# Optimization experiments

Hardware: AMD Instinct MI355X
Metric: run time of the kernel (lower is better)

The kernel has to match this reference:

```python
import jax, jax.numpy as jnp
import numpy as np

B, P, N0 = 8, 32, 10000
K, HIDP = 8, 4
HIDR = 4 * K * HIDP + K   # 136 = backbone output channels
HEADS = 2
E = 160000


def _conv_bn(x, w, b, g, be, dil):
    # x: [B,1,P,N0]; w: [k,1,ks,1]; valid conv along time with dilation dil, then BatchNorm2d (batch stats)
    y = jax.lax.conv_general_dilated(x, w, (1, 1), 'VALID', rhs_dilation=(dil, 1),
                                     dimension_numbers=('NCHW', 'OIHW', 'NCHW'))
    y = y + b[None, :, None, None]
    mu = jnp.mean(y, axis=(0, 2, 3), keepdims=True)
    var = jnp.var(y, axis=(0, 2, 3), keepdims=True)
    return g[None, :, None, None] * (y - mu) * jax.lax.rsqrt(var + 1e-5) + be[None, :, None, None]


def _branch(x, w, b, g, be, dil, pool):
    y = _conv_bn(x, w, b, g, be, dil)
    if pool:  # AdaptiveMaxPool2d((HIDP, N0)): pools only the time axis (node axis already N0)
        T = y.shape[2]
        y = jnp.stack([jnp.max(y[:, :, (i * T) // HIDP: -((-(i + 1) * T) // HIDP), :], axis=2)
                       for i in range(HIDP)], axis=2)
    return y.reshape(y.shape[0], -1, y.shape[-1])  # [B, k*hidP or k, N0]


def _backbone(x, pl1, pl2, pp1, pp2, pg):
    x = x.reshape(-1, 1, P, N0)
    parts = [_branch(x, *pl1, 1, True), _branch(x, *pl2, 1, True),   # local: ks 3,5 dil 1
             _branch(x, *pp1, 2, True), _branch(x, *pp2, 2, True),   # periodic: ks 3,5 dil 2
             _branch(x, *pg, 1, False)]                               # global: ks P, no pool
    return jnp.tanh(jnp.concatenate(parts, axis=1).transpose(0, 2, 1))  # [B, N0, HIDR]


def _gat(xn, W, a_src, a_dst, bias, src, dst, heads, out_ch):
    # PyG GATConv: linear (no bias) -> per-head additive attention -> segment softmax over dst -> scatter-sum
    n = xn.shape[0]
    h = (xn @ W).reshape(n, heads, out_ch)                              # [N,H,C]
    al = jax.nn.leaky_relu(jnp.sum(h * a_src, -1)[src] + jnp.sum(h * a_dst, -1)[dst], 0.2)  # [E',H]
    amax = jax.ops.segment_max(al, dst, num_segments=n)
    ex = jnp.exp(al - amax[dst])
    coef = ex / (jax.ops.segment_sum(ex, dst, num_segments=n)[dst] + 1e-16)
    out = jax.ops.segment_sum(coef[:, :, None] * h[src], dst, num_segments=n)  # [N,H,C]
    return out.reshape(n, heads * out_ch) + bias


def setup_inputs() -> dict:
    key = jax.random.key(0)
    ks = iter(jax.random.split(key, 64))
    nrm = lambda *s: jax.random.normal(next(ks), s, jnp.float32) * 0.05
    d = {"x": jax.random.normal(next(ks), (B, P, N0), jnp.float32)}
    for nm, ksz in (("l1", 3), ("l2", 5), ("p1", 3), ("p2", 5), ("g", P)):
        d["w_" + nm] = nrm(K, 1, ksz, 1)
        d["b_" + nm] = nrm(K)
        d["g_" + nm] = jnp.ones((K,), jnp.float32)
        d["be_" + nm] = jnp.zeros((K,), jnp.float32)
    d["W1"] = nrm(HIDR, HEADS * HIDR); d["as1"] = nrm(HEADS, HIDR); d["ad1"] = nrm(HEADS, HIDR); d["bb1"] = nrm(HEADS * HIDR)
    d["W2"] = nrm(HEADS * HIDR, HIDR); d["as2"] = nrm(1, HIDR); d["ad2"] = nrm(1, HIDR); d["bb2"] = nrm(HIDR)
    d["Wo"] = nrm(2 * HIDR, HIDR); d["bo"] = nrm(HIDR)
    d["Wo2"] = nrm(HIDR, 1); d["bo2"] = nrm(1)
    d["edge_index"] = jax.random.randint(next(ks), (2, E), 0, N0, jnp.int32)
    return d


def reference(x, w_l1, b_l1, g_l1, be_l1, w_l2, b_l2, g_l2, be_l2,
              w_p1, b_p1, g_p1, be_p1, w_p2, b_p2, g_p2, be_p2,
              w_g, b_g, g_g, be_g,
              W1, as1, ad1, bb1, W2, as2, ad2, bb2, Wo, bo, Wo2, bo2, edge_index):
    feat = _backbone(x, (w_l1, b_l1, g_l1, be_l1), (w_l2, b_l2, g_l2, be_l2),
                     (w_p1, b_p1, g_p1, be_p1), (w_p2, b_p2, g_p2, be_p2),
                     (w_g, b_g, g_g, be_g))                                  # [B,N0,HIDR]
    loop = jnp.arange(N0, dtype=edge_index.dtype)                            # GATConv add_self_loops=True
    src = jnp.concatenate([edge_index[0], loop])
    dst = jnp.concatenate([edge_index[1], loop])
    # original loops GATConv per batch item over shared edge_index; vmap is the batched equivalent
    g1 = jax.vmap(lambda f: _gat(f, W1, as1, ad1, bb1, src, dst, HEADS, HIDR))(feat)  # [B,N0,2*HIDR]
    g2 = jax.vmap(lambda f: _gat(f, W2, as2, ad2, bb2, src, dst, 1, HIDR))(g1)        # [B,N0,HIDR]
    ns = jax.nn.leaky_relu(jnp.concatenate([g2, feat], axis=-1))             # dropout is identity at eval
    res = jax.nn.leaky_relu(ns @ Wo + bo)
    return (res @ Wo2 + bo2)[..., 0]                                         # [B,N0]
```

## Files before the change

kernel.cpp:

```cpp
#include <hip/hip_runtime.h>
#include <hip/hip_bf16.h>
#include <math.h>

typedef unsigned short u16;
typedef unsigned int   u32;
typedef short v8s __attribute__((ext_vector_type(8)));
typedef float v4f __attribute__((ext_vector_type(4)));
typedef float v2f __attribute__((ext_vector_type(2)));
#define DEV static __device__ __forceinline__

DEV float u2f(u16 u){ union{u32 i; float f;} v; v.i = ((u32)u)<<16; return v.f; }
DEV u16   f2u(float f){ union{float ff; u32 i;} v; v.ff = f; u32 r = v.i + 0x7fffu + ((v.i>>16)&1u); return (u16)(r>>16); }
DEV float lrelu02(float x){ return x > 0.f ? x : 0.2f*x; }
DEV float lrelu01(float x){ return x > 0.f ? x : 0.01f*x; }
DEV float fast_tanh(float x){
  float cx = fminf(fmaxf(x, -15.f), 15.f);
  float e = __expf(2.f*cx);
  return (e - 1.f) * __builtin_amdgcn_rcpf(e + 1.f);
}
DEV float wred_sum(float v){
  #pragma unroll
  for (int o = 32; o > 0; o >>= 1) v += __shfl_xor(v, o, 64);
  return v;
}
DEV float wred_max32(float v){
  #pragma unroll
  for (int o = 16; o > 0; o >>= 1) v = fmaxf(v, __shfl_xor(v, o, 64));
  return v;
}
DEV float wred_sum32(float v){
  #pragma unroll
  for (int o = 16; o > 0; o >>= 1) v += __shfl_xor(v, o, 64);
  return v;
}
DEV v2f unpack2(u32 w){
  v2f r;
  r.x = __uint_as_float(w << 16);
  r.y = __uint_as_float(w & 0xffff0000u);
  return r;
}

constexpr int B_   = 8;
constexpr int P_   = 32;
constexpr int N0_  = 10000;
constexpr int NODES = B_ * N0_;
constexpr int E_   = 160000;
constexpr int NE_  = E_ + N0_;

__global__ void __launch_bounds__(256) k_setup(int* __restrict__ zbase,
    const float* __restrict__ Wo, u16* __restrict__ WoT,
    const float* __restrict__ W1, const float* __restrict__ W2, u16* __restrict__ W12T,
    const float* __restrict__ as1, const float* __restrict__ ad1,
    float* __restrict__ va1s, float* __restrict__ va1d,
    const float* __restrict__ as2, const float* __restrict__ ad2,
    const float* __restrict__ bb1,
    float* __restrict__ v2ss, float* __restrict__ v2dd,
    float* __restrict__ cc, float* __restrict__ b12)
{
  __shared__ float l2s[272], l2d[272];
  int blk = blockIdx.x, tid = threadIdx.x;
  if (blk < 79){ int i = blk*256 + tid; if (i < 20080) zbase[i] = 0; return; }
  blk -= 79;
  if (blk < 180){
    int i = blk*256 + tid; if (i >= 144*320) return;
    int n = i/320, k = i - n*320; float v = 0.f;
    if (n < 136){
      if (k < 136) v = Wo[(size_t)k*136 + n];
      else if (k >= 160 && k < 296) v = Wo[(size_t)(k-24)*136 + n];
    }
    WoT[i] = f2u(v); return;
  }
  blk -= 180;
  if (blk < 162){
    int i = blk*256 + tid; if (i >= 144*288) return;
    int n = i/288, kk = i - n*288; float v = 0.f;
    if (n < 136 && kk < 272){
      int hh = kk/136, k = kk - hh*136;
      for (int c = 0; c < 136; c++)
        v = fmaf(W1[(size_t)k*272 + hh*136 + c], W2[(size_t)(hh*136+c)*136 + n], v);
    }
    W12T[i] = f2u(v); return;
  }
  blk -= 162;
  if (blk < 2){
    int t = blk*256 + tid; if (t >= 272) return;
    int hh = t/136, k = t - hh*136; float s = 0.f, d = 0.f;
    for (int c = 0; c < 136; c++){
      float w = W1[(size_t)k*272 + hh*136 + c];
      s = fmaf(w, as1[hh*136+c], s);
      d = fmaf(w, ad1[hh*136+c], d);
    }
    va1s[t] = s; va1d[t] = d; return;
  }
  blk -= 2;
  {
    for (int m = tid; m < 272; m += 256){
      float vs = 0.f, vd = 0.f;
      for (int n2 = 0; n2 < 136; n2++){
        float w2 = W2[(size_t)m*136 + n2];
        vs = fmaf(w2, as2[n2], vs);
        vd = fmaf(w2, ad2[n2], vd);
      }
      l2s[m] = vs; l2d[m] = vd;
    }
    __syncthreads();
    int t0 = blk*256 + tid;
    if (t0 < 272){
      int hh = t0/136, k = t0 - hh*136; float s = 0.f, d = 0.f;
      for (int c = 0; c < 136; c++){
        float w = W1[(size_t)k*272 + hh*136 + c];
        s = fmaf(w, l2s[hh*136+c], s);
        d = fmaf(w, l2d[hh*136+c], d);
      }
      v2ss[t0] = s; v2dd[t0] = d;
    }
    if (blk == 1){
      if (tid < 64){
        float s = 0.f, d = 0.f;
        for (int m = tid; m < 272; m += 64){
          s = fmaf(bb1[m], l2s[m], s);
          d = fmaf(bb1[m], l2d[m], d);
        }
        s = wred_sum(s); d = wred_sum(d);
        if (tid == 0){ cc[0] = s; cc[1] = d; }
      } else if (tid < 200){
        int n2 = tid - 64; float v = 0.f;
        for (int m = 0; m < 272; m++) v = fmaf(bb1[m], W2[(size_t)m*136 + n2], v);
        b12[n2] = v;
      }
    }
  }
}

DEV void load_convw(float* lw, const float* wl1, const float* wl2, const float* wp1,
                    const float* wp2, const float* wg, int tid, int nth){
  for (int i = tid; i < 384; i += nth){
    float v;
    if      (i < 24)  v = wl1[i];
    else if (i < 64)  v = wl2[i-24];
    else if (i < 88)  v = wp1[i-64];
    else if (i < 128) v = wp2[i-88];
    else              v = wg [i-128];
    lw[i] = v;
  }
}

template<int KS,int DIL,int T>
DEV void conv_stats(const float* xc, const float* wk, float& s, float& q){
  #pragma unroll
  for (int t = 0; t < T; t++){
    float v = 0.f;
    #pragma unroll
    for (int j = 0; j < KS; j++) v = fmaf(wk[j], xc[t + j*DIL], v);
    s += v; q = fmaf(v, v, q);
  }
}

__global__ void __launch_bounds__(256) k_bn_stats(
    const float* __restrict__ x,
    const float* __restrict__ wl1, const float* __restrict__ wl2,
    const float* __restrict__ wp1, const float* __restrict__ wp2,
    const float* __restrict__ wg,
    float* __restrict__ gsum, float* __restrict__ gsq)
{
  __shared__ float lw[384];
  __shared__ float lacc[80];
  const int tid = threadIdx.x;
  load_convw(lw, wl1, wl2, wp1, wp2, wg, tid, 256);
  if (tid < 80) lacc[tid] = 0.f;
  __syncthreads();

  const int lane = tid & 63, wv = tid >> 6;
  const int nodeLocal = (wv >> 1)*64 + lane;
  const int half = wv & 1;
  const int gid = blockIdx.x*128 + nodeLocal;
  float xc[P_];
  if (gid < NODES){
    int b = gid / N0_, n = gid - b*N0_;
    const float* xp = x + (size_t)b*P_*N0_ + n;
    #pragma unroll
    for (int p = 0; p < P_; p++) xc[p] = xp[(size_t)p*N0_];
  } else {
    #pragma unroll
    for (int p = 0; p < P_; p++) xc[p] = 0.f;
  }

  auto red = [&](int ch, float s, float q){
    #pragma unroll
    for (int o = 32; o > 0; o >>= 1){ s += __shfl_down(s,o,64); q += __shfl_down(q,o,64); }
    if (lane == 0){ atomicAdd(&lacc[ch], s); atomicAdd(&lacc[40+ch], q); }
  };

  if (half == 0){
    #pragma unroll
    for (int k = 0; k < 8; k++){ float s=0,q=0; conv_stats<3,1,30>(xc, lw      + k*3 , s,q); red(k,     s,q); }
    #pragma unroll
    for (int k = 0; k < 8; k++){ float s=0,q=0; conv_stats<5,1,28>(xc, lw + 24 + k*5 , s,q); red(8+k,   s,q); }
  } else {
    #pragma unroll
    for (int k = 0; k < 8; k++){ float s=0,q=0; conv_stats<3,2,28>(xc, lw + 64 + k*3 , s,q); red(16+k,  s,q); }
    #pragma unroll
    for (int k = 0; k < 8; k++){ float s=0,q=0; conv_stats<5,2,24>(xc, lw + 88 + k*5 , s,q); red(24+k,  s,q); }
    #pragma unroll
    for (int k = 0; k < 8; k++){ float s=0,q=0; conv_stats<32,1,1>(xc, lw + 128+ k*32, s,q); red(32+k,  s,q); }
  }

  __syncthreads();
  if (tid < 40)      atomicAdd(&gsum[tid],    lacc[tid]);
  else if (tid < 80) atomicAdd(&gsq [tid-40], lacc[tid]);
}

__global__ void k_count(const int* __restrict__ ei, int* __restrict__ counts,
                        const float* __restrict__ gsum, const float* __restrict__ gsq,
                        float* __restrict__ sA, float* __restrict__ sB,
                        const float* g0, const float* g1, const float* g2, const float* g3, const float* g4,
                        const float* e0, const float* e1, const float* e2, const float* e3, const float* e4){
  if (blockIdx.x == 665){
    int t = threadIdx.x;
    if (t >= 40) return;
    int bi = t >> 3, k = t & 7;
    const int Ts[5] = {30,28,28,24,1};
    float cnt  = (float)NODES * (float)Ts[bi];
    float mean = gsum[t] / cnt;
    float var  = gsq[t] / cnt - mean*mean;
    const float* gp = bi==0?g0: bi==1?g1: bi==2?g2: bi==3?g3: g4;
    const float* ep = bi==0?e0: bi==1?e1: bi==2?e2: bi==3?e3: e4;
    float a = gp[k] * rsqrtf(fmaxf(var, 0.f) + 1e-5f);
    sA[t] = a;
    sB[t] = ep[k] - a*mean;
    return;
  }
  int e = blockIdx.x*blockDim.x + threadIdx.x;
  if (e >= NE_) return;
  int dst = (e < E_) ? ei[E_ + e] : (e - E_);
  atomicAdd(&counts[dst], 1);
}

__global__ void __launch_bounds__(1024) k_scan_perm(const int* __restrict__ counts,
                                                    int* __restrict__ offs,
                                                    int* __restrict__ perm){
  __shared__ int part[1024];
  __shared__ int hist[129];
  __shared__ int base[129];
  int t = threadIdx.x;
  if (blockIdx.x == 0){
    int loc[10]; int s = 0;
    #pragma unroll
    for (int i = 0; i < 10; i++){
      int idx = t*10 + i;
      int c = (idx < N0_) ? counts[idx] : 0;
      loc[i] = s; s += c;
    }
    part[t] = s;
    __syncthreads();
    for (int o = 1; o < 1024; o <<= 1){
      int v = (t >= o) ? part[t-o] : 0;
      __syncthreads();
      part[t] += v;
      __syncthreads();
    }
    int pre = (t == 0) ? 0 : part[t-1];
    #pragma unroll
    for (int i = 0; i < 10; i++){
      int idx = t*10 + i;
      if (idx < N0_) offs[idx] = pre + loc[i];
    }
    if (t == 0) offs[N0_] = part[1023];
  } else {
    if (t < 129) hist[t] = 0;
    __syncthreads();
    int dloc[10];
    #pragma unroll
    for (int i = 0; i < 10; i++){
      int idx = t*10 + i;
      if (idx < N0_){
        int d = min(counts[idx], 128);
        dloc[i] = d;
        atomicAdd(&hist[d], 1);
      }
    }
    __syncthreads();
    if (t == 0){
      int s = 0;
      for (int b = 0; b <= 128; b++){ base[b] = s; s += hist[b]; }
    }
    __syncthreads();
    #pragma unroll
    for (int i = 0; i < 10; i++){
      int idx = t*10 + i;
      if (idx < N0_){
        int pos = atomicAdd(&base[dloc[i]], 1);
        perm[pos] = idx;
      }
    }
  }
}

__global__ void k_scatter(const int* __restrict__ ei, const int* __restrict__ offs,
                          int* __restrict__ cursor, int* __restrict__ srcl){
  int e = blockIdx.x*blockDim.x + threadIdx.x;
  if (e >= NE_) return;
  int src, dst;
  if (e < E_){ src = ei[e]; dst = ei[E_ + e]; } else { src = dst = e - E_; }
  int pos = atomicAdd(&cursor[dst], 1);
  srcl[offs[dst] + pos] = src;
}

template<int KS,int DIL,int T>
DEV void conv_pool4(const float* xc, const float* wk, float A, float Bc, float* o4){
  float y[T];
  #pragma unroll
  for (int t = 0; t < T; t++){
    float v = 0.f;
    #pragma unroll
    for (int j = 0; j < KS; j++) v = fmaf(wk[j], xc[t + j*DIL], v);
    y[t] = fmaf(A, v, Bc);
  }
  #pragma unroll
  for (int i = 0; i < 4; i++){
    const int lo = (i*T)/4, hi = ((i+1)*T + 3)/4;
    float m = y[lo];
    #pragma unroll
    for (int t = 0; t < T; t++){ if (t > lo && t < hi) m = fmaxf(m, y[t]); }
    o4[i] = m;
  }
}

__global__ void __launch_bounds__(256) k_feat(
    const float* __restrict__ x,
    const float* __restrict__ wl1, const float* __restrict__ wl2,
    const float* __restrict__ wp1, const float* __restrict__ wp2,
    const float* __restrict__ wg,
    const float* __restrict__ sA, const float* __restrict__ sB,
    const float* __restrict__ va1s, const float* __restrict__ va1d,
    u16* __restrict__ feat, u16* __restrict__ featL,
    float* __restrict__ asrc1, float* __restrict__ adst1,
    int base, int m)
{
  __shared__ float lw[384];
  __shared__ float lA[40], lB[40];
  __shared__ float4 lv4[136];
  __shared__ float sdt[128][4];
  const int tid = threadIdx.x;
  load_convw(lw, wl1, wl2, wp1, wp2, wg, tid, 256);
  if (tid < 40){ lA[tid] = sA[tid]; lB[tid] = sB[tid]; }
  for (int i = tid; i < 136; i += 256)
    lv4[i] = make_float4(va1s[i], va1d[i], va1s[136+i], va1d[136+i]);
  __syncthreads();

  const int lane = tid & 63, wv = tid >> 6;
  const int nodeLocal = (wv >> 1)*64 + lane;
  const int half = wv & 1;
  const int nodeIdx = blockIdx.x*128 + nodeLocal;
  const bool act = nodeIdx < m;
  const int gcl = base + (act ? nodeIdx : (m-1));
  int b = gcl / N0_, n = gcl - b*N0_;
  float xc[P_];
  const float* xp = x + (size_t)b*P_*N0_ + n;
  #pragma unroll
  for (int p = 0; p < P_; p++) xc[p] = xp[(size_t)p*N0_];

  float dt[4] = {0.f,0.f,0.f,0.f};
  u32 pk[4], pkl[4];
  u16* orow  = feat  + (size_t)nodeIdx*160;
  u16* olrow = featL + (size_t)nodeIdx*160;
  auto emit = [&](int ch, float v){
    float t = fast_tanh(v);
    float4 vv = lv4[ch];
    dt[0] = fmaf(t, vv.x, dt[0]);
    dt[1] = fmaf(t, vv.y, dt[1]);
    dt[2] = fmaf(t, vv.z, dt[2]);
    dt[3] = fmaf(t, vv.w, dt[3]);
    u16 h  = f2u(t);
    u16 hl = f2u(lrelu01(t));
    int s = ch & 7;
    if ((s & 1) == 0){ pk[s>>1] = h;                pkl[s>>1] = hl; }
    else             { pk[s>>1] |= ((u32)h) << 16;  pkl[s>>1] |= ((u32)hl) << 16; }
    if (s == 7 && act){
      *(uint4*)(orow  + (ch - 7)) = make_uint4(pk[0],pk[1],pk[2],pk[3]);
      *(uint4*)(olrow + (ch - 7)) = make_uint4(pkl[0],pkl[1],pkl[2],pkl[3]);
    }
  };

  float o4[4];
  if (half == 0){
    #pragma unroll
    for (int k = 0; k < 8; k++){
      conv_pool4<3,1,30>(xc, lw + k*3, lA[k], lB[k], o4);
      #pragma unroll
      for (int i = 0; i < 4; i++) emit(k*4+i, o4[i]);
    }
    #pragma unroll
    for (int k = 0; k < 8; k++){
      conv_pool4<5,1,28>(xc, lw + 24 + k*5, lA[8+k], lB[8+k], o4);
      #pragma unroll
      for (int i = 0; i < 4; i++) emit(32 + k*4+i, o4[i]);
    }
  } else {
    #pragma unroll
    for (int k = 0; k < 8; k++){
      conv_pool4<3,2,28>(xc, lw + 64 + k*3, lA[16+k], lB[16+k], o4);
      #pragma unroll
      for (int i = 0; i < 4; i++) emit(64 + k*4+i, o4[i]);
    }
    #pragma unroll
    for (int k = 0; k < 8; k++){
      conv_pool4<5,2,24>(xc, lw + 88 + k*5, lA[24+k], lB[24+k], o4);
      #pragma unroll
      for (int i = 0; i < 4; i++) emit(96 + k*4+i, o4[i]);
    }
    #pragma unroll
    for (int k = 0; k < 8; k++){
      float v = 0.f;
      #pragma unroll
      for (int j = 0; j < 32; j++) v = fmaf(lw[128 + k*32 + j], xc[j], v);
      emit(128 + k, fmaf(lA[32+k], v, lB[32+k]));
    }
  }

  if (half == 1){
    sdt[nodeLocal][0] = dt[0]; sdt[nodeLocal][1] = dt[1];
    sdt[nodeLocal][2] = dt[2]; sdt[nodeLocal][3] = dt[3];
  }
  __syncthreads();
  if (half == 0 && act){
    asrc1[(size_t)nodeIdx*2]   = dt[0] + sdt[nodeLocal][0];
    asrc1[(size_t)nodeIdx*2+1] = dt[2] + sdt[nodeLocal][2];
    adst1[(size_t)nodeIdx*2]   = dt[1] + sdt[nodeLocal][1];
    adst1[(size_t)nodeIdx*2+1] = dt[3] + sdt[nodeLocal][3];
  }
}

template<int MT,int KT1,int KT2,int NT,int EPI,int LR2>
__global__ void __launch_bounds__(256) k_mfma(
    const u16* __restrict__ A1, int sA1,
    const u16* __restrict__ A2, int sA2,
    const u16* __restrict__ BT, int sBT,
    u16* __restrict__ C, int sC, int nbase,
    const float* __restrict__ bias, int m,
    const float* __restrict__ w2v, const float* __restrict__ bo2p, float* __restrict__ fout)
{
  const int wv = threadIdx.x >> 6, lane = threadIdx.x & 63;
  const int quad = lane >> 4, l15 = lane & 15;
  const int mb = blockIdx.x*(MT*64) + wv*(MT*16);
  int ar[MT];
  #pragma unroll
  for (int mt = 0; mt < MT; mt++) ar[mt] = min(mb + mt*16 + l15, m-1);

  v4f acc[MT][NT];
  #pragma unroll
  for (int mt = 0; mt < MT; mt++)
    #pragma unroll
    for (int nt = 0; nt < NT; nt++)
      acc[mt][nt] = (v4f){0.f,0.f,0.f,0.f};

  for (int kt = 0; kt < KT1+KT2; kt++){
    const u16* ab; int sA, koff;
    if (KT2 == 0 || kt < KT1){ ab = A1; sA = sA1; koff = kt*32; }
    else { ab = A2; sA = sA2; koff = (kt-KT1)*32; }
    v8s a[MT];
    #pragma unroll
    for (int mt = 0; mt < MT; mt++)
      a[mt] = *(const v8s*)(ab + (size_t)ar[mt]*sA + koff + quad*8);
    if (KT2 > 0 && LR2 && kt >= KT1){
      #pragma unroll
      for (int mt = 0; mt < MT; mt++)
        #pragma unroll
        for (int j = 0; j < 8; j++){
          float f = u2f((u16)a[mt][j]);
          f = f > 0.f ? f : 0.01f*f;
          a[mt][j] = (short)f2u(f);
        }
    }
    const int kb = kt*32 + quad*8;
    #pragma unroll
    for (int nt = 0; nt < NT; nt++){
      v8s b = *(const v8s*)(BT + (size_t)(nbase + nt*16 + l15)*sBT + kb);
      #pragma unroll
      for (int mt = 0; mt < MT; mt++)
        acc[mt][nt] = __builtin_amdgcn_mfma_f32_16x16x32_bf16(a[mt], b, acc[mt][nt], 0, 0, 0);
    }
  }

  if (EPI == 2){
    const float bo2v = bo2p[0];
    #pragma unroll
    for (int mt = 0; mt < MT; mt++){
      float part[4] = {0.f,0.f,0.f,0.f};
      #pragma unroll
      for (int nt = 0; nt < NT; nt++){
        const int col = nt*16 + l15;
        float wv2 = (col < 136) ? w2v[col] : 0.f;
        float bv  = bias[min(col,135)];
        #pragma unroll
        for (int i = 0; i < 4; i++){
          float xv = lrelu01(acc[mt][nt][i] + bv);
          part[i] = fmaf(xv, wv2, part[i]);
        }
      }
      #pragma unroll
      for (int i = 0; i < 4; i++){
        float v = part[i];
        v += __shfl_xor(v, 1, 64);
        v += __shfl_xor(v, 2, 64);
        v += __shfl_xor(v, 4, 64);
        v += __shfl_xor(v, 8, 64);
        int r = mb + mt*16 + quad*4 + i;
        if (l15 == 0 && r < m) fout[r] = v + bo2v;
      }
    }
    return;
  }

  #pragma unroll
  for (int mt = 0; mt < MT; mt++){
    const int r0 = mb + mt*16 + quad*4;
    #pragma unroll
    for (int nt = 0; nt < NT; nt++){
      const int col = nbase + nt*16 + l15;
      #pragma unroll
      for (int i = 0; i < 4; i++){
        int r = r0 + i;
        if (r < m){
          float xv = acc[mt][nt][i];
          if (EPI == 1){ xv += bias[min(col,135)]; xv = lrelu01(xv); }
          if (EPI == 3){ xv += bias[min(col,135)]; }
          C[(size_t)r*sC + col] = f2u(xv);
        }
      }
    }
  }
}

__global__ void __launch_bounds__(256) k_agg1(const u16* __restrict__ feat,
    const float* __restrict__ asrc, const float* __restrict__ adst,
    const int* __restrict__ offs, const int* __restrict__ srcl,
    const int* __restrict__ perm,
    u16* __restrict__ aggF,
    const float* __restrict__ v2s, const float* __restrict__ v2d,
    const float* __restrict__ cc,
    float* __restrict__ as_out, float* __restrict__ ad_out,
    int cbMask, int cbShift)
{
  __shared__ int4 smeta[4][2][32];
  const int tid = threadIdx.x;
  const int wv = tid >> 6, lane = tid & 63;
  const int half = lane >> 5, l32 = lane & 31;
  const int id = blockIdx.x;
  const int bb = id & cbMask;
  const int q = (id >> cbShift)*4 + wv;
  const int dst = perm[2*q + half];
  const int nbase = bb*N0_;
  const int node = nbase + dst;
  const int start = offs[dst], end = offs[dst+1];
  const int ne = end - start;

  const float ad0 = adst[(size_t)node*2], ad1v = adst[(size_t)node*2+1];
  const char* featB = (const char*)feat;

  v2f m01h0 = {0.f,0.f}, m23h0 = {0.f,0.f};
  v2f m01h1 = {0.f,0.f}, m23h1 = {0.f,0.f};
  v2f r01h0 = {0.f,0.f}, r01h1 = {0.f,0.f};

  auto acc_one = [&](int4 mt){
    const u16* fp = (const u16*)(featB + mt.x);
    float c0 = __int_as_float(mt.y), c1 = __int_as_float(mt.z);
    const uint2 hv = *(const uint2*)(fp + 4*l32);
    v2f f01 = unpack2(hv.x), f23 = unpack2(hv.y);
    v2f cc0 = {c0,c0}, cc1 = {c1,c1};
    m01h0 = __builtin_elementwise_fma(f01, cc0, m01h0);
    m23h0 = __builtin_elementwise_fma(f23, cc0, m23h0);
    m01h1 = __builtin_elementwise_fma(f01, cc1, m01h1);
    m23h1 = __builtin_elementwise_fma(f23, cc1, m23h1);
    if (l32 < 4){
      const u32 hr = *(const u32*)(fp + 128 + 2*l32);
      v2f g01 = unpack2(hr);
      r01h0 = __builtin_elementwise_fma(g01, cc0, r01h0);
      r01h1 = __builtin_elementwise_fma(g01, cc1, r01h1);
    }
  };
  auto acc_four = [&](int4 ma, int4 mb, int4 mc, int4 md){
    const u16* p0 = (const u16*)(featB + ma.x);
    const u16* p1 = (const u16*)(featB + mb.x);
    const u16* p2 = (const u16*)(featB + mc.x);
    const u16* p3 = (const u16*)(featB + md.x);
    const uint2 v0 = *(const uint2*)(p0 + 4*l32);
    const uint2 v1 = *(const uint2*)(p1 + 4*l32);
    const uint2 v2 = *(const uint2*)(p2 + 4*l32);
    const uint2 v3 = *(const uint2*)(p3 + 4*l32);
    u32 q0, q1, q2, q3;
    if (l32 < 4){
      q0 = *(const u32*)(p0 + 128 + 2*l32);
      q1 = *(const u32*)(p1 + 128 + 2*l32);
      q2 = *(const u32*)(p2 + 128 + 2*l32);
      q3 = *(const u32*)(p3 + 128 + 2*l32);
    }
    v2f f01, f23, cA, cB;
    #define EDGE1(vv, qq, mm) \
      f01 = unpack2(vv.x); f23 = unpack2(vv.y); \
      cA = (v2f){__int_as_float(mm.y), __int_as_float(mm.y)}; \
      cB = (v2f){__int_as_float(mm.z), __int_as_float(mm.z)}; \
      m01h0 = __builtin_elementwise_fma(f01, cA, m01h0); \
      m23h0 = __builtin_elementwise_fma(f23, cA, m23h0); \
      m01h1 = __builtin_elementwise_fma(f01, cB, m01h1); \
      m23h1 = __builtin_elementwise_fma(f23, cB, m23h1); \
      if (l32 < 4){ \
        v2f g01 = unpack2(qq); \
        r01h0 = __builtin_elementwise_fma(g01, cA, r01h0); \
        r01h1 = __builtin_elementwise_fma(g01, cB, r01h1); \
      }
    EDGE1(v0, q0, ma)
    EDGE1(v1, q1, mb)
    EDGE1(v2, q2, mc)
    EDGE1(v3, q3, md)
    #undef EDGE1
  };
  auto run_chunk = [&](int cnt){
    const int4* mp = &smeta[wv][half][0];
    int j = 0;
    for (; j + 3 < cnt; j += 4)
      acc_four(mp[j], mp[j+1], mp[j+2], mp[j+3]);
    for (; j < cnt; j++)
      acc_one(mp[j]);
  };

  if (ne <= 32){
    const bool has = l32 < ne;
    const int sn = nbase + (has ? srcl[start + l32] : 0);
    const int offL = sn * 320;
    float al0 = has ? lrelu02(asrc[(size_t)sn*2]   + ad0)  : -1e30f;
    float al1 = has ? lrelu02(asrc[(size_t)sn*2+1] + ad1v) : -1e30f;
    float mm = wred_max32(al0);
    float p0 = has ? __expf(al0 - mm) : 0.f;
    float c0 = p0 * (1.f/(wred_sum32(p0) + 1e-16f));
    mm = wred_max32(al1);
    float p1 = has ? __expf(al1 - mm) : 0.f;
    float c1 = p1 * (1.f/(wred_sum32(p1) + 1e-16f));
    if (has)
      smeta[wv][half][l32] = make_int4(offL, __float_as_int(c0), __float_as_int(c1), 0);
    asm volatile("s_waitcnt lgkmcnt(0)" ::: "memory");
    run_chunk(ne);
  } else {
    float lm0 = -1e30f, lm1 = -1e30f;
    for (int e = start + l32; e < end; e += 32){
      int sn = nbase + srcl[e];
      lm0 = fmaxf(lm0, lrelu02(asrc[(size_t)sn*2]   + ad0));
      lm1 = fmaxf(lm1, lrelu02(asrc[(size_t)sn*2+1] + ad1v));
    }
    float m0 = wred_max32(lm0), m1 = wred_max32(lm1);
    float ls0 = 0.f, ls1 = 0.f;
    for (int e = start + l32; e < end; e += 32){
      int sn = nbase + srcl[e];
      ls0 += __expf(lrelu02(asrc[(size_t)sn*2]   + ad0)  - m0);
      ls1 += __expf(lrelu02(asrc[(size_t)sn*2+1] + ad1v) - m1);
    }
    float si0 = 1.f/(wred_sum32(ls0) + 1e-16f);
    float si1 = 1.f/(wred_sum32(ls1) + 1e-16f);
    for (int cs = start; cs < end; cs += 32){
      int cnt = min(32, end - cs);
      bool has = l32 < cnt;
      int sn = nbase + (has ? srcl[cs + l32] : 0);
      int offL = sn * 320;
      float c0 = 0.f, c1 = 0.f;
      if (has){
        c0 = __expf(lrelu02(asrc[(size_t)sn*2]   + ad0)  - m0) * si0;
        c1 = __expf(lrelu02(asrc[(size_t)sn*2+1] + ad1v) - m1) * si1;
      }
      if (has)
        smeta[wv][half][l32] = make_int4(offL, __float_as_int(c0), __float_as_int(c1), 0);
      asm volatile("s_waitcnt lgkmcnt(0)" ::: "memory");
      run_chunk(cnt);
    }
  }

  u16* outp = aggF + (size_t)node*288;
  {
    ushort4 s0; s0.x=f2u(m01h0.x); s0.y=f2u(m01h0.y); s0.z=f2u(m23h0.x); s0.w=f2u(m23h0.y);
    *(ushort4*)(outp + 4*l32) = s0;
    ushort4 s1; s1.x=f2u(m01h1.x); s1.y=f2u(m01h1.y); s1.z=f2u(m23h1.x); s1.w=f2u(m23h1.y);
    *(ushort4*)(outp + 136 + 4*l32) = s1;
    if (l32 < 4){
      ushort2 t0; t0.x=f2u(r01h0.x); t0.y=f2u(r01h0.y);
      *(ushort2*)(outp + 128 + 2*l32) = t0;
      ushort2 t1; t1.x=f2u(r01h1.x); t1.y=f2u(r01h1.y);
      *(ushort2*)(outp + 136 + 128 + 2*l32) = t1;
    }
  }
  {
    int c = 4*l32;
    float s = m01h0.x*v2s[c] + m01h0.y*v2s[c+1] + m23h0.x*v2s[c+2] + m23h0.y*v2s[c+3]
            + m01h1.x*v2s[136+c] + m01h1.y*v2s[136+c+1] + m23h1.x*v2s[136+c+2] + m23h1.y*v2s[136+c+3];
    float d = m01h0.x*v2d[c] + m01h0.y*v2d[c+1] + m23h0.x*v2d[c+2] + m23h0.y*v2d[c+3]
            + m01h1.x*v2d[136+c] + m01h1.y*v2d[136+c+1] + m23h1.x*v2d[136+c+2] + m23h1.y*v2d[136+c+3];
    if (l32 < 4){
      int cr = 128 + 2*l32;
      s += r01h0.x*v2s[cr] + r01h0.y*v2s[cr+1] + r01h1.x*v2s[136+cr] + r01h1.y*v2s[136+cr+1];
      d += r01h0.x*v2d[cr] + r01h0.y*v2d[cr+1] + r01h1.x*v2d[136+cr] + r01h1.y*v2d[136+cr+1];
    }
    s = wred_sum32(s); d = wred_sum32(d);
    if (l32 == 0){ as_out[node] = s + cc[0]; ad_out[node] = d + cc[1]; }
  }
}

__global__ void __launch_bounds__(256) k_agg2(const u16* __restrict__ h, int sh,
    const float* __restrict__ asrc, const float* __restrict__ adst,
    const int* __restrict__ offs, const int* __restrict__ srcl,
    const int* __restrict__ perm,
    const float* __restrict__ bias, u16* __restrict__ outp0, int so,
    int cbMask, int cbShift)
{
  __shared__ int2 smeta[4][2][32];
  const int tid = threadIdx.x;
  const int wv = tid >> 6, lane = tid & 63;
  const int half = lane >> 5, l32 = lane & 31;
  const int id = blockIdx.x;
  const int bb = id & cbMask;
  const int q = (id >> cbShift)*4 + wv;
  const int dst = perm[2*q + half];
  const int nbase = bb*N0_;
  const int node = nbase + dst;
  const int start = offs[dst], end = offs[dst+1];
  const int ne = end - start;
  const int bstride = 2*sh;

  const float adh = adst[node];
  const char* hB = (const char*)h;

  v2f a01 = {0.f,0.f}, a23 = {0.f,0.f}, r01 = {0.f,0.f};

  auto acc_one = [&](int2 mt){
    const u16* hp = (const u16*)(hB + mt.x);
    float c0 = __int_as_float(mt.y);
    const uint2 hv = *(const uint2*)(hp + 4*l32);
    v2f cc0 = {c0,c0};
    a01 = __builtin_elementwise_fma(unpack2(hv.x), cc0, a01);
    a23 = __builtin_elementwise_fma(unpack2(hv.y), cc0, a23);
    if (l32 < 4){
      const u32 hr = *(const u32*)(hp + 128 + 2*l32);
      r01 = __builtin_elementwise_fma(unpack2(hr), cc0, r01);
    }
  };
  auto acc_four = [&](int2 ma, int2 mb, int2 mc, int2 md){
    const u16* p0 = (const u16*)(hB + ma.x);
    const u16* p1 = (const u16*)(hB + mb.x);
    const u16* p2 = (const u16*)(hB + mc.x);
    const u16* p3 = (const u16*)(hB + md.x);
    const uint2 v0 = *(const uint2*)(p0 + 4*l32);
    const uint2 v1 = *(const uint2*)(p1 + 4*l32);
    const uint2 v2 = *(const uint2*)(p2 + 4*l32);
    const uint2 v3 = *(const uint2*)(p3 + 4*l32);
    u32 q0, q1, q2, q3;
    if (l32 < 4){
      q0 = *(const u32*)(p0 + 128 + 2*l32);
      q1 = *(const u32*)(p1 + 128 + 2*l32);
      q2 = *(const u32*)(p2 + 128 + 2*l32);
      q3 = *(const u32*)(p3 + 128 + 2*l32);
    }
    v2f cc;
    #define EDGE2(vv, qq, mm) \
      cc = (v2f){__int_as_float(mm.y), __int_as_float(mm.y)}; \
      a01 = __builtin_elementwise_fma(unpack2(vv.x), cc, a01); \
      a23 = __builtin_elementwise_fma(unpack2(vv.y), cc, a23); \
      if (l32 < 4) r01 = __builtin_elementwise_fma(unpack2(qq), cc, r01);
    EDGE2(v0, q0, ma)
    EDGE2(v1, q1, mb)
    EDGE2(v2, q2, mc)
    EDGE2(v3, q3, md)
    #undef EDGE2
  };
  auto run_chunk = [&](int cnt){
    const int2* mp = &smeta[wv][half][0];
    int j = 0;
    for (; j + 3 < cnt; j += 4)
      acc_four(mp[j], mp[j+1], mp[j+2], mp[j+3]);
    for (; j < cnt; j++)
      acc_one(mp[j]);
  };

  if (ne <= 32){
    const bool has = l32 < ne;
    const int sn = nbase + (has ? srcl[start + l32] : 0);
    const int offL = sn * bstride;
    float al = has ? lrelu02(asrc[sn] + adh) : -1e30f;
    float m = wred_max32(al);
    float p = has ? __expf(al - m) : 0.f;
    float c0 = p * (1.f/(wred_sum32(p) + 1e-16f));
    if (has)
      smeta[wv][half][l32] = make_int2(offL, __float_as_int(c0));
    asm volatile("s_waitcnt lgkmcnt(0)" ::: "memory");
    run_chunk(ne);
  } else {
    float lm = -1e30f;
    for (int e = start + l32; e < end; e += 32){
      int sn = nbase + srcl[e];
      lm = fmaxf(lm, lrelu02(asrc[sn] + adh));
    }
    float m = wred_max32(lm);
    float ls = 0.f;
    for (int e = start + l32; e < end; e += 32){
      int sn = nbase + srcl[e];
      ls += __expf(lrelu02(asrc[sn] + adh) - m);
    }
    float si = 1.f/(wred_sum32(ls) + 1e-16f);
    for (int cs = start; cs < end; cs += 32){
      int cnt = min(32, end - cs);
      bool has = l32 < cnt;
      int sn = nbase + (has ? srcl[cs + l32] : 0);
      int offL = sn * bstride;
      float c0 = has ? __expf(lrelu02(asrc[sn] + adh) - m) * si : 0.f;
      if (has)
        smeta[wv][half][l32] = make_int2(offL, __float_as_int(c0));
      asm volatile("s_waitcnt lgkmcnt(0)" ::: "memory");
      run_chunk(cnt);
    }
  }

  u16* outp = outp0 + (size_t)node*so;
  {
    int c = 4*l32;
    ushort4 st;
    st.x = f2u(lrelu01(a01.x + bias[c]));
    st.y = f2u(lrelu01(a01.y + bias[c+1]));
    st.z = f2u(lrelu01(a23.x + bias[c+2]));
    st.w = f2u(lrelu01(a23.y + bias[c+3]));
    *(ushort4*)(outp + c) = st;
    if (l32 < 4){
      int cr = 128 + 2*l32;
      ushort2 sr;
      sr.x = f2u(lrelu01(r01.x + bias[cr]));
      sr.y = f2u(lrelu01(r01.y + bias[cr+1]));
      *(ushort2*)(outp + cr) = sr;
    }
  }
}

extern "C" void kernel_launch(void* const* d_in, const int* in_sizes, int n_in,
                              void* d_out, int out_size, void* d_ws, size_t ws_size,
                              hipStream_t stream)
{
  (void)in_sizes; (void)n_in; (void)out_size;
  const float* x    = (const float*)d_in[0];
  const float* wl1  = (const float*)d_in[1];
  const float* gl1  = (const float*)d_in[3];
  const float* bel1 = (const float*)d_in[4];
  const float* wl2  = (const float*)d_in[5];
  const float* gl2  = (const float*)d_in[7];
  const float* bel2 = (const float*)d_in[8];
  const float* wp1  = (const float*)d_in[9];
  const float* gp1  = (const float*)d_in[11];
  const float* bep1 = (const float*)d_in[12];
  const float* wp2  = (const float*)d_in[13];
  const float* gp2  = (const float*)d_in[15];
  const float* bep2 = (const float*)d_in[16];
  const float* wg   = (const float*)d_in[17];
  const float* gg   = (const float*)d_in[19];
  const float* beg  = (const float*)d_in[20];
  const float* W1   = (const float*)d_in[21];
  const float* as1  = (const float*)d_in[22];
  const float* ad1  = (const float*)d_in[23];
  const float* bb1  = (const float*)d_in[24];
  const float* W2   = (const float*)d_in[25];
  const float* as2  = (const float*)d_in[26];
  const float* ad2  = (const float*)d_in[27];
  const float* bb2  = (const float*)d_in[28];
  const float* Wo   = (const float*)d_in[29];
  const float* bo   = (const float*)d_in[30];
  const float* Wo2  = (const float*)d_in[31];
  const float* bo2  = (const float*)d_in[32];
  const int*   ei   = (const int*)d_in[33];

  const size_t STATIC_BYTES = 1250000;
  int nc = 1;
  while (nc < 8 && STATIC_BYTES + (size_t)1880*(NODES/nc) > ws_size) nc <<= 1;
  const int CB = B_/nc, CN = CB*N0_;
  int cbShift = 0; while ((1 << cbShift) < CB) cbShift++;
  const int cbMask = CB - 1;

  char* wsb = (char*)d_ws; size_t off = 0;
  auto alloc = [&](size_t nbytes)->void*{
    void* p = wsb + off; off = (off + nbytes + 255) & ~(size_t)255; return p;
  };
  int*   zbase  = (int*)  alloc(20080*sizeof(int));
  float* gsum   = (float*)zbase;
  float* gsq    = gsum + 40;
  int*   counts = zbase + 80;
  int*   cursor = counts + 10000;
  float* sA     = (float*)alloc(40*sizeof(float));
  float* sB     = (float*)alloc(40*sizeof(float));
  int*   offs   = (int*)  alloc(10001*sizeof(int));
  int*   srcl   = (int*)  alloc((size_t)NE_*sizeof(int));
  int*   perm   = (int*)  alloc((size_t)N0_*sizeof(int));
  u16*   W12T   = (u16*)  alloc((size_t)144*288*2);
  u16*   WoT    = (u16*)  alloc((size_t)144*320*2);
  float* va1s   = (float*)alloc(272*sizeof(float));
  float* va1d   = (float*)alloc(272*sizeof(float));
  float* v2ss   = (float*)alloc(272*sizeof(float));
  float* v2dd   = (float*)alloc(272*sizeof(float));
  float* ccv    = (float*)alloc(2*sizeof(float));
  float* b12    = (float*)alloc(136*sizeof(float));
  u16*   feat   = (u16*)  alloc((size_t)CN*160*2);
  u16*   featL  = (u16*)  alloc((size_t)CN*160*2);
  u16*   aggF   = (u16*)  alloc((size_t)CN*288*2);
  u16*   h2     = (u16*)  alloc((size_t)CN*144*2);
  u16*   g2l    = (u16*)  alloc((size_t)CN*160*2);
  float* asrc1  = (float*)alloc((size_t)CN*2*sizeof(float));
  float* adst1  = (float*)alloc((size_t)CN*2*sizeof(float));
  float* asrc2  = (float*)alloc((size_t)CN*sizeof(float));
  float* adst2  = (float*)alloc((size_t)CN*sizeof(float));

  k_setup<<<425,256,0,stream>>>(zbase, Wo, WoT, W1, W2, W12T,
                                as1, ad1, va1s, va1d, as2, ad2, bb1,
                                v2ss, v2dd, ccv, b12);

  k_bn_stats<<<625,256,0,stream>>>(x, wl1,wl2,wp1,wp2,wg, gsum, gsq);

  k_count  <<<666,256,0,stream>>>(ei, counts, gsum, gsq, sA, sB,
                                  gl1,gl2,gp1,gp2,gg, bel1,bel2,bep1,bep2,beg);
  k_scan_perm<<<2,1024,0,stream>>>(counts, offs, perm);
  k_scatter<<<665,256,0,stream>>>(ei, offs, cursor, srcl);

  const int gxm = (CN + 127)/128;
  const int gx2 = (CN + 127)/128;
  const int aggB = 1250*CB;
  for (int c = 0; c < nc; c++){
    const int base = c*CN;

    k_feat<<<gx2,256,0,stream>>>(x, wl1,wl2,wp1,wp2,wg, sA, sB, va1s, va1d,
                                 feat, featL, asrc1, adst1, base, CN);

    k_agg1<<<aggB,256,0,stream>>>(feat, asrc1, adst1, offs, srcl, perm, aggF,
                                  v2ss, v2dd, ccv, asrc2, adst2, cbMask, cbShift);

    k_mfma<2,9,0,9,3,0><<<gxm,256,0,stream>>>(aggF,288, (const u16*)0,0, W12T,288, h2,144, 0, b12, CN,
                                              (const float*)0,(const float*)0,(float*)0);

    k_agg2<<<aggB,256,0,stream>>>(h2,144, asrc2, adst2, offs, srcl, perm, bb2, g2l,160,
                                  cbMask, cbShift);

    k_mfma<2,5,5,9,2,0><<<gxm,256,0,stream>>>(g2l,160, featL,160, WoT,320, (u16*)0,0, 0, bo, CN,
                                              Wo2, bo2, (float*)d_out + base);
  }
}
```

Before: 457.7 us.

## Split half-warp across edge pairs with 16-byte gathers in GAT aggregation

The aggregation kernels now have each 32-lane half-warp work on two edges at a time. Each 16-lane group gathers a full 136-channel row with 16-byte loads, and the two partial sums are combined with a cross-lane shuffle at the end. Odd edge counts are padded with a zero-coefficient sentinel entry in shared memory. Destination nodes are also taken from the end of the permutation, presumably so the heaviest-degree nodes are scheduled first. This aims to cut the number of load instructions per edge and improve memory-level parallelism, at the cost of more accumulator registers and the extra shuffle reduction.

```diff
diff --git a/kernel.cpp b/kernel.cpp
--- a/kernel.cpp
+++ b/kernel.cpp
@@ -11,6 +11,7 @@
 
 DEV float u2f(u16 u){ union{u32 i; float f;} v; v.i = ((u32)u)<<16; return v.f; }
 DEV u16   f2u(float f){ union{float ff; u32 i;} v; v.ff = f; u32 r = v.i + 0x7fffu + ((v.i>>16)&1u); return (u16)(r>>16); }
+DEV u32   pack2(v2f v){ return (u32)f2u(v.x) | ((u32)f2u(v.y) << 16); }
 DEV float lrelu02(float x){ return x > 0.f ? x : 0.2f*x; }
 DEV float lrelu01(float x){ return x > 0.f ? x : 0.01f*x; }
 DEV float fast_tanh(float x){
@@ -542,14 +543,15 @@
     float* __restrict__ as_out, float* __restrict__ ad_out,
     int cbMask, int cbShift)
 {
-  __shared__ int4 smeta[4][2][32];
+  __shared__ int4 smeta[4][2][33];
   const int tid = threadIdx.x;
   const int wv = tid >> 6, lane = tid & 63;
   const int half = lane >> 5, l32 = lane & 31;
+  const int g = l32 >> 4, li = l32 & 15;
   const int id = blockIdx.x;
   const int bb = id & cbMask;
   const int q = (id >> cbShift)*4 + wv;
-  const int dst = perm[2*q + half];
+  const int dst = perm[N0_ - 1 - (2*q + half)];
   const int nbase = bb*N0_;
   const int node = nbase + dst;
   const int start = offs[dst], end = offs[dst+1];
@@ -558,70 +560,46 @@
   const float ad0 = adst[(size_t)node*2], ad1v = adst[(size_t)node*2+1];
   const char* featB = (const char*)feat;
 
-  v2f m01h0 = {0.f,0.f}, m23h0 = {0.f,0.f};
-  v2f m01h1 = {0.f,0.f}, m23h1 = {0.f,0.f};
-  v2f r01h0 = {0.f,0.f}, r01h1 = {0.f,0.f};
-
-  auto acc_one = [&](int4 mt){
+  v2f mh0[4], mh1[4], rh0[2], rh1[2];
+  #pragma unroll
+  for (int k = 0; k < 4; k++){ mh0[k] = (v2f){0.f,0.f}; mh1[k] = (v2f){0.f,0.f}; }
+  #pragma unroll
+  for (int k = 0; k < 2; k++){ rh0[k] = (v2f){0.f,0.f}; rh1[k] = (v2f){0.f,0.f}; }
+
+  auto pair_step = [&](int4 mt){
     const u16* fp = (const u16*)(featB + mt.x);
-    float c0 = __int_as_float(mt.y), c1 = __int_as_float(mt.z);
-    const uint2 hv = *(const uint2*)(fp + 4*l32);
-    v2f f01 = unpack2(hv.x), f23 = unpack2(hv.y);
-    v2f cc0 = {c0,c0}, cc1 = {c1,c1};
-    m01h0 = __builtin_elementwise_fma(f01, cc0, m01h0);
-    m23h0 = __builtin_elementwise_fma(f23, cc0, m23h0);
-    m01h1 = __builtin_elementwise_fma(f01, cc1, m01h1);
-    m23h1 = __builtin_elementwise_fma(f23, cc1, m23h1);
-    if (l32 < 4){
-      const u32 hr = *(const u32*)(fp + 128 + 2*l32);
-      v2f g01 = unpack2(hr);
-      r01h0 = __builtin_elementwise_fma(g01, cc0, r01h0);
-      r01h1 = __builtin_elementwise_fma(g01, cc1, r01h1);
-    }
-  };
-  auto acc_four = [&](int4 ma, int4 mb, int4 mc, int4 md){
-    const u16* p0 = (const u16*)(featB + ma.x);
-    const u16* p1 = (const u16*)(featB + mb.x);
-    const u16* p2 = (const u16*)(featB + mc.x);
-    const u16* p3 = (const u16*)(featB + md.x);
-    const uint2 v0 = *(const uint2*)(p0 + 4*l32);
-    const uint2 v1 = *(const uint2*)(p1 + 4*l32);
-    const uint2 v2 = *(const uint2*)(p2 + 4*l32);
-    const uint2 v3 = *(const uint2*)(p3 + 4*l32);
-    u32 q0, q1, q2, q3;
-    if (l32 < 4){
-      q0 = *(const u32*)(p0 + 128 + 2*l32);
-      q1 = *(const u32*)(p1 + 128 + 2*l32);
-      q2 = *(const u32*)(p2 + 128 + 2*l32);
-      q3 = *(const u32*)(p3 + 128 + 2*l32);
-    }
-    v2f f01, f23, cA, cB;
-    #define EDGE1(vv, qq, mm) \
-      f01 = unpack2(vv.x); f23 = unpack2(vv.y); \
-      cA = (v2f){__int_as_float(mm.y), __int_as_float(mm.y)}; \
-      cB = (v2f){__int_as_float(mm.z), __int_as_float(mm.z)}; \
-      m01h0 = __builtin_elementwise_fma(f01, cA, m01h0); \
-      m23h0 = __builtin_elementwise_fma(f23, cA, m23h0); \
-      m01h1 = __builtin_elementwise_fma(f01, cB, m01h1); \
-      m23h1 = __builtin_elementwise_fma(f23, cB, m23h1); \
-      if (l32 < 4){ \
-        v2f g01 = unpack2(qq); \
-        r01h0 = __builtin_elementwise_fma(g01, cA, r01h0); \
-        r01h1 = __builtin_elementwise_fma(g01, cB, r01h1); \
-      }
-    EDGE1(v0, q0, ma)
-    EDGE1(v1, q1, mb)
-    EDGE1(v2, q2, mc)
-    EDGE1(v3, q3, md)
-    #undef EDGE1
+    const uint4 hv = *(const uint4*)(fp + 8*li);
+    v2f cA = {__int_as_float(mt.y), __int_as_float(mt.y)};
+    v2f cB = {__int_as_float(mt.z), __int_as_float(mt.z)};
+    v2f f0 = unpack2(hv.x), f1 = unpack2(hv.y), f2 = unpack2(hv.z), f3 = unpack2(hv.w);
+    mh0[0] = __builtin_elementwise_fma(f0, cA, mh0[0]);
+    mh0[1] = __builtin_elementwise_fma(f1, cA, mh0[1]);
+    mh0[2] = __builtin_elementwise_fma(f2, cA, mh0[2]);
+    mh0[3] = __builtin_elementwise_fma(f3, cA, mh0[3]);
+    mh1[0] = __builtin_elementwise_fma(f0, cB, mh1[0]);
+    mh1[1] = __builtin_elementwise_fma(f1, cB, mh1[1]);
+    mh1[2] = __builtin_elementwise_fma(f2, cB, mh1[2]);
+    mh1[3] = __builtin_elementwise_fma(f3, cB, mh1[3]);
+    if (li < 2){
+      const uint2 hr = *(const uint2*)(fp + 128 + 4*li);
+      v2f g0 = unpack2(hr.x), g1 = unpack2(hr.y);
+      rh0[0] = __builtin_elementwise_fma(g0, cA, rh0[0]);
+      rh0[1] = __builtin_elementwise_fma(g1, cA, rh0[1]);
+      rh1[0] = __builtin_elementwise_fma(g0, cB, rh1[0]);
+      rh1[1] = __builtin_elementwise_fma(g1, cB, rh1[1]);
+    }
   };
   auto run_chunk = [&](int cnt){
     const int4* mp = &smeta[wv][half][0];
+    const int cntE = cnt + (cnt & 1);
     int j = 0;
-    for (; j + 3 < cnt; j += 4)
-      acc_four(mp[j], mp[j+1], mp[j+2], mp[j+3]);
-    for (; j < cnt; j++)
-      acc_one(mp[j]);
+    for (; j + 3 < cntE; j += 4){
+      int4 a = mp[j+g];
+      int4 b = mp[j+2+g];
+      pair_step(a);
+      pair_step(b);
+    }
+    if (j < cntE) pair_step(mp[j+g]);
   };
 
   if (ne <= 32){
@@ -638,6 +616,8 @@
     float c1 = p1 * (1.f/(wred_sum32(p1) + 1e-16f));
     if (has)
       smeta[wv][half][l32] = make_int4(offL, __float_as_int(c0), __float_as_int(c1), 0);
+    if (l32 == ne)
+      smeta[wv][half][l32] = make_int4(0, 0, 0, 0);
     asm volatile("s_waitcnt lgkmcnt(0)" ::: "memory");
     run_chunk(ne);
   } else {
@@ -668,38 +648,69 @@
       }
       if (has)
         smeta[wv][half][l32] = make_int4(offL, __float_as_int(c0), __float_as_int(c1), 0);
+      if (l32 == cnt)
+        smeta[wv][half][l32] = make_int4(0, 0, 0, 0);
       asm volatile("s_waitcnt lgkmcnt(0)" ::: "memory");
       run_chunk(cnt);
     }
   }
 
+  auto comb = [&](v2f& v){
+    v.x += __shfl_xor(v.x, 16, 64);
+    v.y += __shfl_xor(v.y, 16, 64);
+  };
+  #pragma unroll
+  for (int k = 0; k < 4; k++){ comb(mh0[k]); comb(mh1[k]); }
+  #pragma unroll
+  for (int k = 0; k < 2; k++){ comb(rh0[k]); comb(rh1[k]); }
+
   u16* outp = aggF + (size_t)node*288;
-  {
-    ushort4 s0; s0.x=f2u(m01h0.x); s0.y=f2u(m01h0.y); s0.z=f2u(m23h0.x); s0.w=f2u(m23h0.y);
-    *(ushort4*)(outp + 4*l32) = s0;
-    ushort4 s1; s1.x=f2u(m01h1.x); s1.y=f2u(m01h1.y); s1.z=f2u(m23h1.x); s1.w=f2u(m23h1.y);
-    *(ushort4*)(outp + 136 + 4*l32) = s1;
-    if (l32 < 4){
-      ushort2 t0; t0.x=f2u(r01h0.x); t0.y=f2u(r01h0.y);
-      *(ushort2*)(outp + 128 + 2*l32) = t0;
-      ushort2 t1; t1.x=f2u(r01h1.x); t1.y=f2u(r01h1.y);
-      *(ushort2*)(outp + 136 + 128 + 2*l32) = t1;
-    }
-  }
-  {
-    int c = 4*l32;
-    float s = m01h0.x*v2s[c] + m01h0.y*v2s[c+1] + m23h0.x*v2s[c+2] + m23h0.y*v2s[c+3]
-            + m01h1.x*v2s[136+c] + m01h1.y*v2s[136+c+1] + m23h1.x*v2s[136+c+2] + m23h1.y*v2s[136+c+3];
-    float d = m01h0.x*v2d[c] + m01h0.y*v2d[c+1] + m23h0.x*v2d[c+2] + m23h0.y*v2d[c+3]
-            + m01h1.x*v2d[136+c] + m01h1.y*v2d[136+c+1] + m23h1.x*v2d[136+c+2] + m23h1.y*v2d[136+c+3];
-    if (l32 < 4){
-      int cr = 128 + 2*l32;
-      s += r01h0.x*v2s[cr] + r01h0.y*v2s[cr+1] + r01h1.x*v2s[136+cr] + r01h1.y*v2s[136+cr+1];
-      d += r01h0.x*v2d[cr] + r01h0.y*v2d[cr+1] + r01h1.x*v2d[136+cr] + r01h1.y*v2d[136+cr+1];
-    }
-    s = wred_sum32(s); d = wred_sum32(d);
-    if (l32 == 0){ as_out[node] = s + cc[0]; ad_out[node] = d + cc[1]; }
-  }
+  if (g == 0){
+    uint4 st = make_uint4(pack2(mh0[0]), pack2(mh0[1]), pack2(mh0[2]), pack2(mh0[3]));
+    *(uint4*)(outp + 8*li) = st;
+    if (li < 2){
+      ushort4 sr;
+      sr.x = f2u(rh0[0].x); sr.y = f2u(rh0[0].y);
+      sr.z = f2u(rh0[1].x); sr.w = f2u(rh0[1].y);
+      *(ushort4*)(outp + 128 + 4*li) = sr;
+    }
+  } else {
+    uint4 st = make_uint4(pack2(mh1[0]), pack2(mh1[1]), pack2(mh1[2]), pack2(mh1[3]));
+    *(uint4*)(outp + 136 + 8*li) = st;
+    if (li < 2){
+      ushort4 sr;
+      sr.x = f2u(rh1[0].x); sr.y = f2u(rh1[0].y);
+      sr.z = f2u(rh1[1].x); sr.w = f2u(rh1[1].y);
+      *(ushort4*)(outp + 136 + 128 + 4*li) = sr;
+    }
+  }
+
+  float s = 0.f, d = 0.f;
+  if (g == 0){
+    int c = 8*li;
+    s = mh0[0].x*v2s[c]   + mh0[0].y*v2s[c+1] + mh0[1].x*v2s[c+2] + mh0[1].y*v2s[c+3]
+      + mh0[2].x*v2s[c+4] + mh0[2].y*v2s[c+5] + mh0[3].x*v2s[c+6] + mh0[3].y*v2s[c+7];
+    d = mh0[0].x*v2d[c]   + mh0[0].y*v2d[c+1] + mh0[1].x*v2d[c+2] + mh0[1].y*v2d[c+3]
+      + mh0[2].x*v2d[c+4] + mh0[2].y*v2d[c+5] + mh0[3].x*v2d[c+6] + mh0[3].y*v2d[c+7];
+    if (li < 2){
+      int cr = 128 + 4*li;
+      s += rh0[0].x*v2s[cr] + rh0[0].y*v2s[cr+1] + rh0[1].x*v2s[cr+2] + rh0[1].y*v2s[cr+3];
+      d += rh0[0].x*v2d[cr] + rh0[0].y*v2d[cr+1] + rh0[1].x*v2d[cr+2] + rh0[1].y*v2d[cr+3];
+    }
+  } else {
+    int c = 136 + 8*li;
+    s = mh1[0].x*v2s[c]   + mh1[0].y*v2s[c+1] + mh1[1].x*v2s[c+2] + mh1[1].y*v2s[c+3]
+      + mh1[2].x*v2s[c+4] + mh1[2].y*v2s[c+5] + mh1[3].x*v2s[c+6] + mh1[3].y*v2s[c+7];
+    d = mh1[0].x*v2d[c]   + mh1[0].y*v2d[c+1] + mh1[1].x*v2d[c+2] + mh1[1].y*v2d[c+3]
+      + mh1[2].x*v2d[c+4] + mh1[2].y*v2d[c+5] + mh1[3].x*v2d[c+6] + mh1[3].y*v2d[c+7];
+    if (li < 2){
+      int cr = 136 + 128 + 4*li;
+      s += rh1[0].x*v2s[cr] + rh1[0].y*v2s[cr+1] + rh1[1].x*v2s[cr+2] + rh1[1].y*v2s[cr+3];
+      d += rh1[0].x*v2d[cr] + rh1[0].y*v2d[cr+1] + rh1[1].x*v2d[cr+2] + rh1[1].y*v2d[cr+3];
+    }
+  }
+  s = wred_sum32(s); d = wred_sum32(d);
+  if (l32 == 0){ as_out[node] = s + cc[0]; ad_out[node] = d + cc[1]; }
 }
 
 __global__ void __launch_bounds__(256) k_agg2(const u16* __restrict__ h, int sh,
@@ -709,14 +720,15 @@
     const float* __restrict__ bias, u16* __restrict__ outp0, int so,
     int cbMask, int cbShift)
 {
-  __shared__ int2 smeta[4][2][32];
+  __shared__ int2 smeta[4][2][33];
   const int tid = threadIdx.x;
   const int wv = tid >> 6, lane = tid & 63;
   const int half = lane >> 5, l32 = lane & 31;
+  const int g = l32 >> 4, li = l32 & 15;
   const int id = blockIdx.x;
   const int bb = id & cbMask;
   const int q = (id >> cbShift)*4 + wv;
-  const int dst = perm[2*q + half];
+  const int dst = perm[N0_ - 1 - (2*q + half)];
   const int nbase = bb*N0_;
   const int node = nbase + dst;
   const int start = offs[dst], end = offs[dst+1];
@@ -726,55 +738,36 @@
   const float adh = adst[node];
   const char* hB = (const char*)h;
 
-  v2f a01 = {0.f,0.f}, a23 = {0.f,0.f}, r01 = {0.f,0.f};
-
-  auto acc_one = [&](int2 mt){
+  v2f ma[4], ra[2];
+  #pragma unroll
+  for (int k = 0; k < 4; k++) ma[k] = (v2f){0.f,0.f};
+  ra[0] = (v2f){0.f,0.f}; ra[1] = (v2f){0.f,0.f};
+
+  auto pair_step = [&](int2 mt){
     const u16* hp = (const u16*)(hB + mt.x);
-    float c0 = __int_as_float(mt.y);
-    const uint2 hv = *(const uint2*)(hp + 4*l32);
-    v2f cc0 = {c0,c0};
-    a01 = __builtin_elementwise_fma(unpack2(hv.x), cc0, a01);
-    a23 = __builtin_elementwise_fma(unpack2(hv.y), cc0, a23);
-    if (l32 < 4){
-      const u32 hr = *(const u32*)(hp + 128 + 2*l32);
-      r01 = __builtin_elementwise_fma(unpack2(hr), cc0, r01);
-    }
-  };
-  auto acc_four = [&](int2 ma, int2 mb, int2 mc, int2 md){
-    const u16* p0 = (const u16*)(hB + ma.x);
-    const u16* p1 = (const u16*)(hB + mb.x);
-    const u16* p2 = (const u16*)(hB + mc.x);
-    const u16* p3 = (const u16*)(hB + md.x);
-    const uint2 v0 = *(const uint2*)(p0 + 4*l32);
-    const uint2 v1 = *(const uint2*)(p1 + 4*l32);
-    const uint2 v2 = *(const uint2*)(p2 + 4*l32);
-    const uint2 v3 = *(const uint2*)(p3 + 4*l32);
-    u32 q0, q1, q2, q3;
-    if (l32 < 4){
-      q0 = *(const u32*)(p0 + 128 + 2*l32);
-      q1 = *(const u32*)(p1 + 128 + 2*l32);
-      q2 = *(const u32*)(p2 + 128 + 2*l32);
-      q3 = *(const u32*)(p3 + 128 + 2*l32);
-    }
-    v2f cc;
-    #define EDGE2(vv, qq, mm) \
-      cc = (v2f){__int_as_float(mm.y), __int_as_float(mm.y)}; \
-      a01 = __builtin_elementwise_fma(unpack2(vv.x), cc, a01); \
-      a23 = __builtin_elementwise_fma(unpack2(vv.y), cc, a23); \
-      if (l32 < 4) r01 = __builtin_elementwise_fma(unpack2(qq), cc, r01);
-    EDGE2(v0, q0, ma)
-    EDGE2(v1, q1, mb)
-    EDGE2(v2, q2, mc)
-    EDGE2(v3, q3, md)
-    #undef EDGE2
+    const uint4 hv = *(const uint4*)(hp + 8*li);
+    v2f cA = {__int_as_float(mt.y), __int_as_float(mt.y)};
+    ma[0] = __builtin_elementwise_fma(unpack2(hv.x), cA, ma[0]);
+    ma[1] = __builtin_elementwise_fma(unpack2(hv.y), cA, ma[1]);
+    ma[2] = __builtin_elementwise_fma(unpack2(hv.z), cA, ma[2]);
+    ma[3] = __builtin_elementwise_fma(unpack2(hv.w), cA, ma[3]);
+    if (li < 2){
+      const uint2 hr = *(const uint2*)(hp + 128 + 4*li);
+      ra[0] = __builtin_elementwise_fma(unpack2(hr.x), cA, ra[0]);
+      ra[1] = __builtin_elementwise_fma(unpack2(hr.y), cA, ra[1]);
+    }
   };
   auto run_chunk = [&](int cnt){
     const int2* mp = &smeta[wv][half][0];
+    const int cntE = cnt + (cnt & 1);
     int j = 0;
-    for (; j + 3 < cnt; j += 4)
-      acc_four(mp[j], mp[j+1], mp[j+2], mp[j+3]);
-    for (; j < cnt; j++)
-      acc_one(mp[j]);
+    for (; j + 3 < cntE; j += 4){
+      int2 a = mp[j+g];
+      int2 b = mp[j+2+g];
+      pair_step(a);
+      pair_step(b);
+    }
+    if (j < cntE) pair_step(mp[j+g]);
   };
 
   if (ne <= 32){
@@ -787,6 +780,8 @@
     float c0 = p * (1.f/(wred_sum32(p) + 1e-16f));
     if (has)
       smeta[wv][half][l32] = make_int2(offL, __float_as_int(c0));
+    if (l32 == ne)
+      smeta[wv][half][l32] = make_int2(0, 0);
     asm volatile("s_waitcnt lgkmcnt(0)" ::: "memory");
     run_chunk(ne);
   } else {
@@ -810,26 +805,43 @@
       float c0 = has ? __expf(lrelu02(asrc[sn] + adh) - m) * si : 0.f;
       if (has)
         smeta[wv][half][l32] = make_int2(offL, __float_as_int(c0));
+      if (l32 == cnt)
+        smeta[wv][half][l32] = make_int2(0, 0);
       asm volatile("s_waitcnt lgkmcnt(0)" ::: "memory");
       run_chunk(cnt);
     }
   }
 
+  auto comb = [&](v2f& v){
+    v.x += __shfl_xor(v.x, 16, 64);
+    v.y += __shfl_xor(v.y, 16, 64);
+  };
+  #pragma unroll
+  for (int k = 0; k < 4; k++) comb(ma[k]);
+  comb(ra[0]); comb(ra[1]);
+
   u16* outp = outp0 + (size_t)node*so;
-  {
-    int c = 4*l32;
-    ushort4 st;
-    st.x = f2u(lrelu01(a01.x + bias[c]));
-    st.y = f2u(lrelu01(a01.y + bias[c+1]));
-    st.z = f2u(lrelu01(a23.x + bias[c+2]));
-    st.w = f2u(lrelu01(a23.y + bias[c+3]));
-    *(ushort4*)(outp + c) = st;
-    if (l32 < 4){
-      int cr = 128 + 2*l32;
-      ushort2 sr;
-      sr.x = f2u(lrelu01(r01.x + bias[cr]));
-      sr.y = f2u(lrelu01(r01.y + bias[cr+1]));
-      *(ushort2*)(outp + cr) = sr;
+  if (g == 0){
+    int c = 8*li;
+    ushort4 s0, s1;
+    s0.x = f2u(lrelu01(ma[0].x + bias[c]));
+    s0.y = f2u(lrelu01(ma[0].y + bias[c+1]));
+    s0.z = f2u(lrelu01(ma[1].x + bias[c+2]));
+    s0.w = f2u(lrelu01(ma[1].y + bias[c+3]));
+    s1.x = f2u(lrelu01(ma[2].x + bias[c+4]));
+    s1.y = f2u(lrelu01(ma[2].y + bias[c+5]));
+    s1.z = f2u(lrelu01(ma[3].x + bias[c+6]));
+    s1.w = f2u(lrelu01(ma[3].y + bias[c+7]));
+    *(ushort4*)(outp + c) = s0;
+    *(ushort4*)(outp + c + 4) = s1;
+    if (li < 2){
+      int cr = 128 + 4*li;
+      ushort4 sr;
+      sr.x = f2u(lrelu01(ra[0].x + bias[cr]));
+      sr.y = f2u(lrelu01(ra[0].y + bias[cr+1]));
+      sr.z = f2u(lrelu01(ra[1].x + bias[cr+2]));
+      sr.w = f2u(lrelu01(ra[1].y + bias[cr+3]));
+      *(ushort4*)(outp + cr) = sr;
     }
   }
 }
```

New measurement: 460.7 us. Within noise of the previous version (+0.7%).
